# Kernel tuning notes

Measured on AMD Instinct MI355X. Metric: run time of the kernel, lower is better.

The kernel has to match this reference:

```python
import jax, jax.numpy as jnp
import numpy as np

N = 100000
E = 1600000
IN_CH, HID_CH, OUT_CH = 128, 64, 32


def setup_inputs() -> dict:
    key = jax.random.key(0)
    ks = jax.random.split(key, 6)
    x = jax.random.normal(ks[0], (N, IN_CH), dtype=jnp.float32)
    ei = jax.random.randint(ks[1], (2, E), 0, N, dtype=jnp.int64)
    W1 = jax.random.normal(ks[2], (IN_CH, HID_CH), dtype=jnp.float32) * 0.05
    b1 = jax.random.normal(ks[3], (HID_CH,), dtype=jnp.float32) * 0.05
    W2 = jax.random.normal(ks[4], (HID_CH, OUT_CH), dtype=jnp.float32) * 0.05
    b2 = jax.random.normal(ks[5], (OUT_CH,), dtype=jnp.float32) * 0.05
    return {"x": x, "ei": ei, "W1": W1, "b1": b1, "W2": W2, "b2": b2}


def gcn_layer(x, sa, da, n):
    # degree with self-loops already appended in sa/da
    deg = jax.ops.segment_sum(jnp.ones((sa.shape[0],), x.dtype), da, num_segments=n)
    prod = deg[sa] * deg[da]
    norm = jnp.where(prod > 0, jax.lax.rsqrt(prod), 0.0)  # (deg_s*deg_d)^-0.5, inf->0
    msg = x[sa] * norm[:, None]            # [E+N, C] gather + scale
    return jax.ops.segment_sum(msg, da, num_segments=n)  # scatter_add


def reference(x, ei, W1, b1, W2, b2):
    n = x.shape[0]
    loop = jnp.arange(n, dtype=ei.dtype)
    sa = jnp.concatenate([ei[0], loop])
    da = jnp.concatenate([ei[1], loop])
    h = gcn_layer(x @ W1 + b1, sa, da, n)
    h = jax.nn.relu(h)
    # dropout: eval mode (training=False) -> identity
    return gcn_layer(h @ W2 + b2, sa, da, n)
```

## Files before the change

### kernel.cpp

```cpp
#include <hip/hip_runtime.h>

#define NN 100000
#define NE 1600000
#define IN_CH 128
#define HID_CH 64
#define OUT_CH 32
#define NB2 98
#define CHUNKA 8192
#define NBLKA ((NE + CHUNKA - 1) / CHUNKA)
#define NBLK_GEMM ((NN + 63) / 64)

typedef unsigned short ushort_t;
typedef _Float16 half2_t __attribute__((ext_vector_type(2)));
typedef float f32x2 __attribute__((ext_vector_type(2)));

__device__ inline ushort_t f2bf(float f) {
    union { float f; unsigned u; } v; v.f = f;
    unsigned r = v.u + 0x7fff + ((v.u >> 16) & 1);
    return (ushort_t)(r >> 16);
}
__device__ inline float blo(unsigned u) {
    union { unsigned x; float f; } v; v.x = u << 16; return v.f;
}
__device__ inline float bhi(unsigned u) {
    union { unsigned x; float f; } v; v.x = u & 0xffff0000u; return v.f;
}
__device__ inline unsigned pkh(float a, float b) {
    union { half2_t h; unsigned u; } v;
    v.h[0] = (_Float16)a; v.h[1] = (_Float16)b;
    return v.u;
}
__device__ inline half2_t u2h(unsigned u) {
    union { unsigned u; half2_t h; } v; v.u = u; return v.h;
}
__device__ inline float fdot2(unsigned a, unsigned b, float c) {
#if __has_builtin(__builtin_amdgcn_fdot2)
    return __builtin_amdgcn_fdot2(u2h(a), u2h(b), c, false);
#else
    half2_t ha = u2h(a), hb = u2h(b);
    return c + (float)ha[0] * (float)hb[0] + (float)ha[1] * (float)hb[1];
#endif
}
__device__ inline f32x2 pk_add(f32x2 a, f32x2 b) {
    f32x2 r;
    asm("v_pk_add_f32 %0, %1, %2" : "=v"(r) : "v"(a), "v"(b));
    return r;
}

__global__ __launch_bounds__(256) void k_bhist(const int* __restrict__ da,
                                               int* __restrict__ bcnt,
                                               int* __restrict__ bhall) {
    __shared__ int hist[4][NB2];
    int t = threadIdx.x, w = t >> 6;
    for (int i = t; i < 4 * NB2; i += 256) ((int*)hist)[i] = 0;
    __syncthreads();
    int base = blockIdx.x * CHUNKA;
    for (int i = 0; i < CHUNKA; i += 256) {
        int e = base + i + t;
        if (e < NE) atomicAdd(&hist[w][da[e] >> 10], 1);
    }
    __syncthreads();
    if (t < NB2) {
        int c = hist[0][t] + hist[1][t] + hist[2][t] + hist[3][t];
        bhall[blockIdx.x * NB2 + t] = c;
        if (c) atomicAdd(&bcnt[t], c);
    }
}

__global__ __launch_bounds__(128) void k_bscan(const int* __restrict__ bcnt,
                                               int* __restrict__ bbase,
                                               int* __restrict__ bcur,
                                               int* __restrict__ rowptr) {
    __shared__ int lds[128];
    int t = threadIdx.x;
    int v = (t < NB2) ? bcnt[t] : 0;
    lds[t] = v;
    __syncthreads();
    for (int off = 1; off < 128; off <<= 1) {
        int x = (t >= off) ? lds[t - off] : 0;
        __syncthreads();
        lds[t] += x;
        __syncthreads();
    }
    int excl = lds[t] - v;
    if (t < NB2) { bbase[t] = excl; bcur[t] = excl; }
    if (t == 0) { bbase[NB2] = NE; rowptr[NN] = NE; }
}

__global__ __launch_bounds__(256) void k_bfill(const int* __restrict__ sa,
                                               const int* __restrict__ da,
                                               const int* __restrict__ bhall,
                                               int* __restrict__ bcur,
                                               unsigned* __restrict__ ebuf) {
    __shared__ int lcur[NB2];
    int t = threadIdx.x;
    if (t < NB2) {
        int c = bhall[blockIdx.x * NB2 + t];
        lcur[t] = c ? atomicAdd(&bcur[t], c) : 0;
    }
    __syncthreads();
    int base = blockIdx.x * CHUNKA;
    for (int i = 0; i < CHUNKA; i += 256) {
        int e = base + i + t;
        if (e < NE) {
            int d = da[e];
            int p = atomicAdd(&lcur[d >> 10], 1);
            ebuf[p] = ((unsigned)sa[e] << 10) | (unsigned)(d & 1023);
        }
    }
}

__global__ __launch_bounds__(1024) void k_bcount(const unsigned* __restrict__ ebuf,
                                                 const int* __restrict__ bbase,
                                                 int* __restrict__ rowptr,
                                                 float* __restrict__ rs) {
    __shared__ int cnt[1024];
    __shared__ int scn[1024];
    int b = blockIdx.x, t = threadIdx.x;
    int nb = NN - b * 1024; if (nb > 1024) nb = 1024;
    int beg = bbase[b], end = bbase[b + 1];
    cnt[t] = 0;
    __syncthreads();
    for (int i = beg + t; i < end; i += 1024) atomicAdd(&cnt[ebuf[i] & 1023], 1);
    __syncthreads();
    int v = cnt[t];
    scn[t] = v;
    __syncthreads();
    for (int off = 1; off < 1024; off <<= 1) {
        int x = (t >= off) ? scn[t - off] : 0;
        __syncthreads();
        scn[t] += x;
        __syncthreads();
    }
    int excl = scn[t] - v;
    if (t < nb) {
        rowptr[b * 1024 + t] = beg + excl;
        rs[b * 1024 + t] = rsqrtf((float)(v + 1));
    }
}

#define SWZU1(n, k2) ((n) * 64 + ((k2) ^ ((((n) & 7)) << 2)))
#define SWZ2(n, k) ((n) * 64 + ((k) ^ ((((n) & 7)) << 2)))

__global__ __launch_bounds__(256, 4) void k_scatter_gemm1(
    const unsigned* __restrict__ ebuf, const int* __restrict__ rowptr,
    const int* __restrict__ bbase, int* __restrict__ col,
    const float* __restrict__ x, const float* __restrict__ W1,
    const float* __restrict__ b1, const float* __restrict__ rs,
    ushort_t* __restrict__ xsb) {
    __shared__ unsigned xth[64 * 64];
    __shared__ unsigned w1h[64 * 64];
    __shared__ int cur[1024];
    int t = threadIdx.x;

    if (blockIdx.x < NB2) {
        int b = blockIdx.x;
#pragma unroll
        for (int j = 0; j < 4; ++j) {
            int n = b * 1024 + j * 256 + t;
            cur[j * 256 + t] = (n < NN) ? rowptr[n] : 0;
        }
        int beg = bbase[b], end = bbase[b + 1];
        __syncthreads();
        for (int i = beg + t; i < end; i += 256) {
            unsigned w = ebuf[i];
            int pos = atomicAdd(&cur[w & 1023], 1);
            col[pos] = (int)(w >> 10);
        }
        return;
    }

    int base = (blockIdx.x - NB2) * 64;
#pragma unroll
    for (int i = 0; i < 8; ++i) {
        int flat = i * 1024 + t * 4;
        int node = flat >> 7, k0 = flat & 127;
        int gn = base + node;
        float4 v = make_float4(0.f, 0.f, 0.f, 0.f);
        if (gn < NN) v = *(const float4*)(x + (size_t)gn * IN_CH + k0);
        uint2 pk;
        pk.x = pkh(v.x, v.y);
        pk.y = pkh(v.z, v.w);
        *(uint2*)&xth[SWZU1(node, k0 >> 1)] = pk;
    }
#pragma unroll
    for (int i = 0; i < 16; ++i) {
        int idx = i * 256 + t;
        int k2 = idx >> 6, c = idx & 63;
        float f0 = W1[(2 * k2) * 64 + c];
        float f1 = W1[(2 * k2 + 1) * 64 + c];
        w1h[idx] = pkh(f0, f1);
    }
    __syncthreads();

    int tn = t & 15, tc = t >> 4;
    int c0 = tc * 4;
    float acc[4][4];
#pragma unroll
    for (int a = 0; a < 4; ++a)
#pragma unroll
        for (int b = 0; b < 4; ++b) acc[a][b] = 0.f;

    for (int k2 = 0; k2 < 64; k2 += 2) {
        uint2 xu[4];
#pragma unroll
        for (int jn = 0; jn < 4; ++jn)
            xu[jn] = *(uint2*)&xth[SWZU1(tn + jn * 16, k2)];
        uint4 w0 = *(uint4*)&w1h[(k2 + 0) * 64 + c0];
        uint4 w1 = *(uint4*)&w1h[(k2 + 1) * 64 + c0];
        unsigned wq0[4] = {w0.x, w0.y, w0.z, w0.w};
        unsigned wq1[4] = {w1.x, w1.y, w1.z, w1.w};
#pragma unroll
        for (int jn = 0; jn < 4; ++jn)
#pragma unroll
            for (int jc = 0; jc < 4; ++jc) {
                acc[jn][jc] = fdot2(xu[jn].x, wq0[jc], acc[jn][jc]);
                acc[jn][jc] = fdot2(xu[jn].y, wq1[jc], acc[jn][jc]);
            }
    }

    float4 bb = *(const float4*)&b1[c0];
#pragma unroll
    for (int jn = 0; jn < 4; ++jn) {
        int gn = base + tn + jn * 16;
        if (gn < NN) {
            float r = rs[gn];
            uint2 pk;
            pk.x = (unsigned)f2bf((acc[jn][0] + bb.x) * r) |
                   ((unsigned)f2bf((acc[jn][1] + bb.y) * r) << 16);
            pk.y = (unsigned)f2bf((acc[jn][2] + bb.z) * r) |
                   ((unsigned)f2bf((acc[jn][3] + bb.w) * r) << 16);
            *(uint2*)&xsb[(size_t)gn * HID_CH + c0] = pk;
        }
    }
}

#define ADD8PK(v) do { \
    f32x2 w0_, w1_, w2_, w3_; \
    w0_.x = blo((v).x); w0_.y = bhi((v).x); p0 = pk_add(p0, w0_); \
    w1_.x = blo((v).y); w1_.y = bhi((v).y); p1 = pk_add(p1, w1_); \
    w2_.x = blo((v).z); w2_.y = bhi((v).z); p2 = pk_add(p2, w2_); \
    w3_.x = blo((v).w); w3_.y = bhi((v).w); p3 = pk_add(p3, w3_); } while (0)

__global__ __launch_bounds__(256) void k_agg1(
    const int* __restrict__ rowptr, const int* __restrict__ col,
    const ushort_t* __restrict__ xsb, const float* __restrict__ rs,
    ushort_t* __restrict__ hb) {
    int gid = blockIdx.x * blockDim.x + threadIdx.x;
    int n = gid >> 6;
    if (n >= NN) return;
    int lane = threadIdx.x & 63;
    int g = lane >> 3;
    unsigned c0 = (unsigned)(lane & 7) * 8;
    int beg = rowptr[n], end = rowptr[n + 1];

    f32x2 p0 = {0.f, 0.f}, p1 = {0.f, 0.f}, p2 = {0.f, 0.f}, p3 = {0.f, 0.f};
    if (g == 0) {
        uint4 sv = *(const uint4*)&xsb[(unsigned)n * 64u + c0];
        ADD8PK(sv);
    }

    int i = beg;
    for (; i + 16 <= end; i += 16) {
        int s0 = col[i + g];
        int s1 = col[i + 8 + g];
        uint4 v0 = *(const uint4*)&xsb[(unsigned)s0 * 64u + c0];
        uint4 v1 = *(const uint4*)&xsb[(unsigned)s1 * 64u + c0];
        ADD8PK(v0);
        ADD8PK(v1);
    }
    if (i + 8 <= end) {
        int s0 = col[i + g];
        uint4 v0 = *(const uint4*)&xsb[(unsigned)s0 * 64u + c0];
        ADD8PK(v0);
        i += 8;
    }
    int r = end - i;
    if (g < r) {
        int s0 = col[i + g];
        uint4 v0 = *(const uint4*)&xsb[(unsigned)s0 * 64u + c0];
        ADD8PK(v0);
    }

    float a0 = p0.x, a1 = p0.y, a2 = p1.x, a3 = p1.y;
    float a4 = p2.x, a5 = p2.y, a6 = p3.x, a7 = p3.y;
#pragma unroll
    for (int m = 8; m <= 32; m <<= 1) {
        a0 += __shfl_xor(a0, m); a1 += __shfl_xor(a1, m);
        a2 += __shfl_xor(a2, m); a3 += __shfl_xor(a3, m);
        a4 += __shfl_xor(a4, m); a5 += __shfl_xor(a5, m);
        a6 += __shfl_xor(a6, m); a7 += __shfl_xor(a7, m);
    }

    if (g == 0) {
        float rn = rs[n];
        uint4 pk;
        pk.x = (unsigned)f2bf(fmaxf(a0 * rn, 0.f)) |
               ((unsigned)f2bf(fmaxf(a1 * rn, 0.f)) << 16);
        pk.y = (unsigned)f2bf(fmaxf(a2 * rn, 0.f)) |
               ((unsigned)f2bf(fmaxf(a3 * rn, 0.f)) << 16);
        pk.z = (unsigned)f2bf(fmaxf(a4 * rn, 0.f)) |
               ((unsigned)f2bf(fmaxf(a5 * rn, 0.f)) << 16);
        pk.w = (unsigned)f2bf(fmaxf(a6 * rn, 0.f)) |
               ((unsigned)f2bf(fmaxf(a7 * rn, 0.f)) << 16);
        *(uint4*)&hb[(unsigned)n * 64u + c0] = pk;
    }
}

__global__ __launch_bounds__(256) void k_gemm2(
    const ushort_t* __restrict__ hb, const float* __restrict__ W2,
    const float* __restrict__ b2, const float* __restrict__ rs,
    ushort_t* __restrict__ ysb) {
    __shared__ float ht[64 * 64];
    __shared__ float w2s[64 * 32];
    int t = threadIdx.x;
    int base = blockIdx.x * 64;

#pragma unroll
    for (int i = 0; i < 8; ++i) {
        int uidx = i * 256 + t;
        int node = uidx >> 5, k2 = uidx & 31;
        int gn = base + node;
        unsigned u = 0;
        if (gn < NN) u = *(const unsigned*)&hb[(size_t)gn * HID_CH + k2 * 2];
        float2 f; f.x = blo(u); f.y = bhi(u);
        *(float2*)&ht[SWZ2(node, k2 * 2)] = f;
    }
#pragma unroll
    for (int i = 0; i < 2; ++i) {
        int flat = i * 1024 + t * 4;
        *(float4*)&w2s[flat] = *(const float4*)(W2 + flat);
    }
    __syncthreads();

    int tn = t & 15, tc = t >> 4;
    int c0 = tc * 2;
    float acc[4][2];
#pragma unroll
    for (int a = 0; a < 4; ++a) { acc[a][0] = 0.f; acc[a][1] = 0.f; }

    for (int k0 = 0; k0 < 64; k0 += 4) {
        float xq[4][4], wq[4][2];
#pragma unroll
        for (int j = 0; j < 4; ++j)
            *(float2*)&wq[j][0] = *(float2*)&w2s[(k0 + j) * 32 + c0];
#pragma unroll
        for (int jn = 0; jn < 4; ++jn)
            *(float4*)&xq[jn][0] = *(float4*)&ht[SWZ2(tn + jn * 16, k0)];
#pragma unroll
        for (int jn = 0; jn < 4; ++jn)
#pragma unroll
            for (int j = 0; j < 4; ++j) {
                acc[jn][0] = fmaf(xq[jn][j], wq[j][0], acc[jn][0]);
                acc[jn][1] = fmaf(xq[jn][j], wq[j][1], acc[jn][1]);
            }
    }

    float2 bb = *(const float2*)&b2[c0];
#pragma unroll
    for (int jn = 0; jn < 4; ++jn) {
        int gn = base + tn + jn * 16;
        if (gn < NN) {
            float r = rs[gn];
            unsigned pk = (unsigned)f2bf((acc[jn][0] + bb.x) * r) |
                          ((unsigned)f2bf((acc[jn][1] + bb.y) * r) << 16);
            *(unsigned*)&ysb[(size_t)gn * OUT_CH + c0] = pk;
        }
    }
}

__global__ __launch_bounds__(256) void k_agg2(
    const int* __restrict__ rowptr, const int* __restrict__ col,
    const ushort_t* __restrict__ ysb, const float* __restrict__ rs,
    float* __restrict__ out) {
    int gid = blockIdx.x * blockDim.x + threadIdx.x;
    int n = gid >> 6;
    if (n >= NN) return;
    int lane = threadIdx.x & 63;
    int g = lane >> 2;
    unsigned c0 = (unsigned)(lane & 3) * 8;
    int beg = rowptr[n], end = rowptr[n + 1];

    f32x2 p0 = {0.f, 0.f}, p1 = {0.f, 0.f}, p2 = {0.f, 0.f}, p3 = {0.f, 0.f};
    if (g == 0) {
        uint4 sv = *(const uint4*)&ysb[(unsigned)n * 32u + c0];
        ADD8PK(sv);
    }

    int i = beg;
    for (; i + 16 <= end; i += 16) {
        int s0 = col[i + g];
        uint4 v0 = *(const uint4*)&ysb[(unsigned)s0 * 32u + c0];
        ADD8PK(v0);
    }
    int r = end - i;
    if (g < r) {
        int s0 = col[i + g];
        uint4 v0 = *(const uint4*)&ysb[(unsigned)s0 * 32u + c0];
        ADD8PK(v0);
    }

    float a0 = p0.x, a1 = p0.y, a2 = p1.x, a3 = p1.y;
    float a4 = p2.x, a5 = p2.y, a6 = p3.x, a7 = p3.y;
#pragma unroll
    for (int m = 4; m <= 32; m <<= 1) {
        a0 += __shfl_xor(a0, m); a1 += __shfl_xor(a1, m);
        a2 += __shfl_xor(a2, m); a3 += __shfl_xor(a3, m);
        a4 += __shfl_xor(a4, m); a5 += __shfl_xor(a5, m);
        a6 += __shfl_xor(a6, m); a7 += __shfl_xor(a7, m);
    }

    if (g == 0) {
        float rn = rs[n];
        float4 o0, o1;
        o0.x = a0 * rn; o0.y = a1 * rn; o0.z = a2 * rn; o0.w = a3 * rn;
        o1.x = a4 * rn; o1.y = a5 * rn; o1.z = a6 * rn; o1.w = a7 * rn;
        *(float4*)&out[(size_t)n * OUT_CH + c0] = o0;
        *(float4*)&out[(size_t)n * OUT_CH + c0 + 4] = o1;
    }
}

extern "C" void kernel_launch(void* const* d_in, const int* in_sizes, int n_in,
                              void* d_out, int out_size, void* d_ws, size_t ws_size,
                              hipStream_t stream) {
    const float* x  = (const float*)d_in[0];
    const int*   ei = (const int*)d_in[1];
    const float* W1 = (const float*)d_in[2];
    const float* b1 = (const float*)d_in[3];
    const float* W2 = (const float*)d_in[4];
    const float* b2 = (const float*)d_in[5];
    const int* sa = ei;
    const int* da = ei + NE;

    char* ws = (char*)d_ws;
    size_t off = 0;
    auto alloc = [&](size_t bytes) {
        void* p = ws + off;
        off += (bytes + 255) & ~(size_t)255;
        return p;
    };
    int*      bcnt   = (int*)alloc((size_t)NB2 * 4);
    int*      bbase  = (int*)alloc((size_t)(NB2 + 1) * 4);
    int*      bcur   = (int*)alloc((size_t)NB2 * 4);
    int*      bhall  = (int*)alloc((size_t)NBLKA * NB2 * 4);
    int*      rowptr = (int*)alloc((size_t)(NN + 1) * 4);
    float*    rs     = (float*)alloc((size_t)NN * 4);
    unsigned* ebuf   = (unsigned*)alloc((size_t)NE * 4);
    int*      col    = (int*)alloc((size_t)NE * 4);
    ushort_t* xsb    = (ushort_t*)alloc((size_t)NN * HID_CH * 2);
    ushort_t* hb     = (ushort_t*)alloc((size_t)NN * HID_CH * 2);
    ushort_t* ysb    = (ushort_t*)alloc((size_t)NN * OUT_CH * 2);
    float*    outp   = (float*)d_out;

    const int B = 256;
    hipMemsetAsync(bcnt, 0, (size_t)NB2 * 4, stream);
    k_bhist<<<NBLKA, 256, 0, stream>>>(da, bcnt, bhall);
    k_bscan<<<1, 128, 0, stream>>>(bcnt, bbase, bcur, rowptr);
    k_bfill<<<NBLKA, 256, 0, stream>>>(sa, da, bhall, bcur, ebuf);
    k_bcount<<<NB2, 1024, 0, stream>>>(ebuf, bbase, rowptr, rs);
    k_scatter_gemm1<<<NB2 + NBLK_GEMM, 256, 0, stream>>>(ebuf, rowptr, bbase, col,
                                                         x, W1, b1, rs, xsb);
    k_agg1<<<(NN * 64 + B - 1) / B, B, 0, stream>>>(rowptr, col, xsb, rs, hb);
    k_gemm2<<<NBLK_GEMM, 256, 0, stream>>>(hb, W2, b2, rs, ysb);
    k_agg2<<<(NN * 64 + B - 1) / B, B, 0, stream>>>(rowptr, col, ysb, rs, outp);
}
```

Before: 210.1 us.

## Fuse CSR build and GEMM1 into one cooperative persistent kernel with grid syncs

Replaces the histogram, scan, fill, count and scatter/GEMM1 kernels plus the memset with a single cooperative kernel that uses grid-wide syncs between phases and grid-stride virtual blocks. The aim is to remove launch overhead and the inter-kernel gaps of several small kernels. The bucket totals are now recomputed serially by block 0 from the per-chunk histograms, which drops the global atomics on bcnt. Grid syncs add their own cost, and the GEMM phase now runs with a grid limited by occupancy.

```diff
diff --git a/kernel.cpp b/kernel.cpp
--- a/kernel.cpp
+++ b/kernel.cpp
@@ -1,4 +1,7 @@
 #include <hip/hip_runtime.h>
+#include <hip/hip_cooperative_groups.h>
+
+namespace cg = cooperative_groups;
 
 #define NN 100000
 #define NE 1600000
@@ -9,6 +12,7 @@
 #define CHUNKA 8192
 #define NBLKA ((NE + CHUNKA - 1) / CHUNKA)
 #define NBLK_GEMM ((NN + 63) / 64)
+#define NVB5 (NB2 + NBLK_GEMM)
 
 typedef unsigned short ushort_t;
 typedef _Float16 half2_t __attribute__((ext_vector_type(2)));
@@ -47,190 +51,187 @@
     return r;
 }
 
-__global__ __launch_bounds__(256) void k_bhist(const int* __restrict__ da,
-                                               int* __restrict__ bcnt,
-                                               int* __restrict__ bhall) {
-    __shared__ int hist[4][NB2];
-    int t = threadIdx.x, w = t >> 6;
-    for (int i = t; i < 4 * NB2; i += 256) ((int*)hist)[i] = 0;
-    __syncthreads();
-    int base = blockIdx.x * CHUNKA;
-    for (int i = 0; i < CHUNKA; i += 256) {
-        int e = base + i + t;
-        if (e < NE) atomicAdd(&hist[w][da[e] >> 10], 1);
-    }
-    __syncthreads();
-    if (t < NB2) {
-        int c = hist[0][t] + hist[1][t] + hist[2][t] + hist[3][t];
-        bhall[blockIdx.x * NB2 + t] = c;
-        if (c) atomicAdd(&bcnt[t], c);
-    }
-}
-
-__global__ __launch_bounds__(128) void k_bscan(const int* __restrict__ bcnt,
-                                               int* __restrict__ bbase,
-                                               int* __restrict__ bcur,
-                                               int* __restrict__ rowptr) {
-    __shared__ int lds[128];
-    int t = threadIdx.x;
-    int v = (t < NB2) ? bcnt[t] : 0;
-    lds[t] = v;
-    __syncthreads();
-    for (int off = 1; off < 128; off <<= 1) {
-        int x = (t >= off) ? lds[t - off] : 0;
-        __syncthreads();
-        lds[t] += x;
-        __syncthreads();
-    }
-    int excl = lds[t] - v;
-    if (t < NB2) { bbase[t] = excl; bcur[t] = excl; }
-    if (t == 0) { bbase[NB2] = NE; rowptr[NN] = NE; }
-}
-
-__global__ __launch_bounds__(256) void k_bfill(const int* __restrict__ sa,
-                                               const int* __restrict__ da,
-                                               const int* __restrict__ bhall,
-                                               int* __restrict__ bcur,
-                                               unsigned* __restrict__ ebuf) {
-    __shared__ int lcur[NB2];
-    int t = threadIdx.x;
-    if (t < NB2) {
-        int c = bhall[blockIdx.x * NB2 + t];
-        lcur[t] = c ? atomicAdd(&bcur[t], c) : 0;
-    }
-    __syncthreads();
-    int base = blockIdx.x * CHUNKA;
-    for (int i = 0; i < CHUNKA; i += 256) {
-        int e = base + i + t;
-        if (e < NE) {
-            int d = da[e];
-            int p = atomicAdd(&lcur[d >> 10], 1);
-            ebuf[p] = ((unsigned)sa[e] << 10) | (unsigned)(d & 1023);
-        }
-    }
-}
-
-__global__ __launch_bounds__(1024) void k_bcount(const unsigned* __restrict__ ebuf,
-                                                 const int* __restrict__ bbase,
-                                                 int* __restrict__ rowptr,
-                                                 float* __restrict__ rs) {
-    __shared__ int cnt[1024];
-    __shared__ int scn[1024];
-    int b = blockIdx.x, t = threadIdx.x;
-    int nb = NN - b * 1024; if (nb > 1024) nb = 1024;
-    int beg = bbase[b], end = bbase[b + 1];
-    cnt[t] = 0;
-    __syncthreads();
-    for (int i = beg + t; i < end; i += 1024) atomicAdd(&cnt[ebuf[i] & 1023], 1);
-    __syncthreads();
-    int v = cnt[t];
-    scn[t] = v;
-    __syncthreads();
-    for (int off = 1; off < 1024; off <<= 1) {
-        int x = (t >= off) ? scn[t - off] : 0;
-        __syncthreads();
-        scn[t] += x;
-        __syncthreads();
-    }
-    int excl = scn[t] - v;
-    if (t < nb) {
-        rowptr[b * 1024 + t] = beg + excl;
-        rs[b * 1024 + t] = rsqrtf((float)(v + 1));
-    }
-}
-
 #define SWZU1(n, k2) ((n) * 64 + ((k2) ^ ((((n) & 7)) << 2)))
 #define SWZ2(n, k) ((n) * 64 + ((k) ^ ((((n) & 7)) << 2)))
 
-__global__ __launch_bounds__(256, 4) void k_scatter_gemm1(
-    const unsigned* __restrict__ ebuf, const int* __restrict__ rowptr,
-    const int* __restrict__ bbase, int* __restrict__ col,
+__global__ __launch_bounds__(256, 4) void k_mega(
+    const int* __restrict__ sa, const int* __restrict__ da,
+    int* __restrict__ bhall, int* __restrict__ bbase, int* __restrict__ bcur,
+    int* __restrict__ rowptr, float* __restrict__ rs,
+    unsigned* __restrict__ ebuf, int* __restrict__ col,
     const float* __restrict__ x, const float* __restrict__ W1,
-    const float* __restrict__ b1, const float* __restrict__ rs,
-    ushort_t* __restrict__ xsb) {
-    __shared__ unsigned xth[64 * 64];
-    __shared__ unsigned w1h[64 * 64];
-    __shared__ int cur[1024];
+    const float* __restrict__ b1, ushort_t* __restrict__ xsb) {
+    __shared__ int smem[8192];
+    cg::grid_group grid = cg::this_grid();
     int t = threadIdx.x;
 
-    if (blockIdx.x < NB2) {
-        int b = blockIdx.x;
-#pragma unroll
-        for (int j = 0; j < 4; ++j) {
-            int n = b * 1024 + j * 256 + t;
-            cur[j * 256 + t] = (n < NN) ? rowptr[n] : 0;
-        }
-        int beg = bbase[b], end = bbase[b + 1];
-        __syncthreads();
-        for (int i = beg + t; i < end; i += 256) {
-            unsigned w = ebuf[i];
-            int pos = atomicAdd(&cur[w & 1023], 1);
-            col[pos] = (int)(w >> 10);
-        }
-        return;
-    }
-
-    int base = (blockIdx.x - NB2) * 64;
-#pragma unroll
-    for (int i = 0; i < 8; ++i) {
-        int flat = i * 1024 + t * 4;
-        int node = flat >> 7, k0 = flat & 127;
-        int gn = base + node;
-        float4 v = make_float4(0.f, 0.f, 0.f, 0.f);
-        if (gn < NN) v = *(const float4*)(x + (size_t)gn * IN_CH + k0);
-        uint2 pk;
-        pk.x = pkh(v.x, v.y);
-        pk.y = pkh(v.z, v.w);
-        *(uint2*)&xth[SWZU1(node, k0 >> 1)] = pk;
-    }
-#pragma unroll
-    for (int i = 0; i < 16; ++i) {
-        int idx = i * 256 + t;
-        int k2 = idx >> 6, c = idx & 63;
-        float f0 = W1[(2 * k2) * 64 + c];
-        float f1 = W1[(2 * k2 + 1) * 64 + c];
-        w1h[idx] = pkh(f0, f1);
-    }
-    __syncthreads();
-
-    int tn = t & 15, tc = t >> 4;
-    int c0 = tc * 4;
-    float acc[4][4];
-#pragma unroll
-    for (int a = 0; a < 4; ++a)
-#pragma unroll
-        for (int b = 0; b < 4; ++b) acc[a][b] = 0.f;
-
-    for (int k2 = 0; k2 < 64; k2 += 2) {
-        uint2 xu[4];
-#pragma unroll
-        for (int jn = 0; jn < 4; ++jn)
-            xu[jn] = *(uint2*)&xth[SWZU1(tn + jn * 16, k2)];
-        uint4 w0 = *(uint4*)&w1h[(k2 + 0) * 64 + c0];
-        uint4 w1 = *(uint4*)&w1h[(k2 + 1) * 64 + c0];
-        unsigned wq0[4] = {w0.x, w0.y, w0.z, w0.w};
-        unsigned wq1[4] = {w1.x, w1.y, w1.z, w1.w};
-#pragma unroll
-        for (int jn = 0; jn < 4; ++jn)
-#pragma unroll
-            for (int jc = 0; jc < 4; ++jc) {
-                acc[jn][jc] = fdot2(xu[jn].x, wq0[jc], acc[jn][jc]);
-                acc[jn][jc] = fdot2(xu[jn].y, wq1[jc], acc[jn][jc]);
+    for (int vb = blockIdx.x; vb < NBLKA; vb += gridDim.x) {
+        __syncthreads();
+        for (int i = t; i < 4 * NB2; i += 256) smem[i] = 0;
+        __syncthreads();
+        int base = vb * CHUNKA;
+        int w = t >> 6;
+        for (int i = 0; i < CHUNKA; i += 256) {
+            int e = base + i + t;
+            if (e < NE) atomicAdd(&smem[w * NB2 + (da[e] >> 10)], 1);
+        }
+        __syncthreads();
+        if (t < NB2)
+            bhall[vb * NB2 + t] =
+                smem[t] + smem[NB2 + t] + smem[2 * NB2 + t] + smem[3 * NB2 + t];
+        __syncthreads();
+    }
+    grid.sync();
+
+    if (blockIdx.x == 0) {
+        int v = 0;
+        if (t < NB2)
+            for (int r = 0; r < NBLKA; ++r) v += bhall[r * NB2 + t];
+        smem[t] = v;
+        __syncthreads();
+        for (int off = 1; off < 256; off <<= 1) {
+            int xv = (t >= off) ? smem[t - off] : 0;
+            __syncthreads();
+            smem[t] += xv;
+            __syncthreads();
+        }
+        int excl = smem[t] - v;
+        if (t < NB2) { bbase[t] = excl; bcur[t] = excl; }
+        if (t == 0) { bbase[NB2] = NE; rowptr[NN] = NE; }
+    }
+    grid.sync();
+
+    for (int vb = blockIdx.x; vb < NBLKA; vb += gridDim.x) {
+        __syncthreads();
+        if (t < NB2) {
+            int c = bhall[vb * NB2 + t];
+            smem[t] = c ? atomicAdd(&bcur[t], c) : 0;
+        }
+        __syncthreads();
+        int base = vb * CHUNKA;
+        for (int i = 0; i < CHUNKA; i += 256) {
+            int e = base + i + t;
+            if (e < NE) {
+                int d = da[e];
+                int p = atomicAdd(&smem[d >> 10], 1);
+                ebuf[p] = ((unsigned)sa[e] << 10) | (unsigned)(d & 1023);
             }
-    }
-
-    float4 bb = *(const float4*)&b1[c0];
-#pragma unroll
-    for (int jn = 0; jn < 4; ++jn) {
-        int gn = base + tn + jn * 16;
-        if (gn < NN) {
-            float r = rs[gn];
+        }
+    }
+    grid.sync();
+
+    for (int vb = blockIdx.x; vb < NB2; vb += gridDim.x) {
+        __syncthreads();
+        *(int4*)&smem[t * 4] = make_int4(0, 0, 0, 0);
+        __syncthreads();
+        int beg = bbase[vb], end = bbase[vb + 1];
+        for (int i = beg + t; i < end; i += 256)
+            atomicAdd(&smem[ebuf[i] & 1023], 1);
+        __syncthreads();
+        int4 v4 = *(int4*)&smem[t * 4];
+        int s = v4.x + v4.y + v4.z + v4.w;
+        smem[1024 + t] = s;
+        __syncthreads();
+        for (int off = 1; off < 256; off <<= 1) {
+            int xv = (t >= off) ? smem[1024 + t - off] : 0;
+            __syncthreads();
+            smem[1024 + t] += xv;
+            __syncthreads();
+        }
+        int excl = smem[1024 + t] - s;
+        int p0 = beg + excl;
+        int p1 = p0 + v4.x;
+        int p2 = p1 + v4.y;
+        int p3 = p2 + v4.z;
+        int n = vb * 1024 + t * 4;
+        if (n + 0 < NN) { rowptr[n + 0] = p0; rs[n + 0] = rsqrtf((float)(v4.x + 1)); }
+        if (n + 1 < NN) { rowptr[n + 1] = p1; rs[n + 1] = rsqrtf((float)(v4.y + 1)); }
+        if (n + 2 < NN) { rowptr[n + 2] = p2; rs[n + 2] = rsqrtf((float)(v4.z + 1)); }
+        if (n + 3 < NN) { rowptr[n + 3] = p3; rs[n + 3] = rsqrtf((float)(v4.w + 1)); }
+    }
+    grid.sync();
+
+    unsigned* xth = (unsigned*)smem;
+    unsigned* w1h = (unsigned*)smem + 4096;
+    for (int vb = blockIdx.x; vb < NVB5; vb += gridDim.x) {
+        __syncthreads();
+        if (vb < NB2) {
+#pragma unroll
+            for (int j = 0; j < 4; ++j) {
+                int n = vb * 1024 + j * 256 + t;
+                smem[j * 256 + t] = (n < NN) ? rowptr[n] : 0;
+            }
+            int beg = bbase[vb], end = bbase[vb + 1];
+            __syncthreads();
+            for (int i = beg + t; i < end; i += 256) {
+                unsigned w = ebuf[i];
+                int pos = atomicAdd(&smem[w & 1023], 1);
+                col[pos] = (int)(w >> 10);
+            }
+            continue;
+        }
+        int base = (vb - NB2) * 64;
+#pragma unroll
+        for (int i = 0; i < 8; ++i) {
+            int flat = i * 1024 + t * 4;
+            int node = flat >> 7, k0 = flat & 127;
+            int gn = base + node;
+            float4 v = make_float4(0.f, 0.f, 0.f, 0.f);
+            if (gn < NN) v = *(const float4*)(x + (size_t)gn * IN_CH + k0);
             uint2 pk;
-            pk.x = (unsigned)f2bf((acc[jn][0] + bb.x) * r) |
-                   ((unsigned)f2bf((acc[jn][1] + bb.y) * r) << 16);
-            pk.y = (unsigned)f2bf((acc[jn][2] + bb.z) * r) |
-                   ((unsigned)f2bf((acc[jn][3] + bb.w) * r) << 16);
-            *(uint2*)&xsb[(size_t)gn * HID_CH + c0] = pk;
+            pk.x = pkh(v.x, v.y);
+            pk.y = pkh(v.z, v.w);
+            *(uint2*)&xth[SWZU1(node, k0 >> 1)] = pk;
+        }
+#pragma unroll
+        for (int i = 0; i < 16; ++i) {
+            int idx = i * 256 + t;
+            int k2 = idx >> 6, c = idx & 63;
+            float f0 = W1[(2 * k2) * 64 + c];
+            float f1 = W1[(2 * k2 + 1) * 64 + c];
+            w1h[idx] = pkh(f0, f1);
+        }
+        __syncthreads();
+
+        int tn = t & 15, tc = t >> 4;
+        int c0 = tc * 4;
+        float acc[4][4];
+#pragma unroll
+        for (int a = 0; a < 4; ++a)
+#pragma unroll
+            for (int b = 0; b < 4; ++b) acc[a][b] = 0.f;
+
+        for (int k2 = 0; k2 < 64; k2 += 2) {
+            uint2 xu[4];
+#pragma unroll
+            for (int jn = 0; jn < 4; ++jn)
+                xu[jn] = *(uint2*)&xth[SWZU1(tn + jn * 16, k2)];
+            uint4 w0 = *(uint4*)&w1h[(k2 + 0) * 64 + c0];
+            uint4 w1 = *(uint4*)&w1h[(k2 + 1) * 64 + c0];
+            unsigned wq0[4] = {w0.x, w0.y, w0.z, w0.w};
+            unsigned wq1[4] = {w1.x, w1.y, w1.z, w1.w};
+#pragma unroll
+            for (int jn = 0; jn < 4; ++jn)
+#pragma unroll
+                for (int jc = 0; jc < 4; ++jc) {
+                    acc[jn][jc] = fdot2(xu[jn].x, wq0[jc], acc[jn][jc]);
+                    acc[jn][jc] = fdot2(xu[jn].y, wq1[jc], acc[jn][jc]);
+                }
+        }
+
+        float4 bb = *(const float4*)&b1[c0];
+#pragma unroll
+        for (int jn = 0; jn < 4; ++jn) {
+            int gn = base + tn + jn * 16;
+            if (gn < NN) {
+                float r = rs[gn];
+                uint2 pk;
+                pk.x = (unsigned)f2bf((acc[jn][0] + bb.x) * r) |
+                       ((unsigned)f2bf((acc[jn][1] + bb.y) * r) << 16);
+                pk.y = (unsigned)f2bf((acc[jn][2] + bb.z) * r) |
+                       ((unsigned)f2bf((acc[jn][3] + bb.w) * r) << 16);
+                *(uint2*)&xsb[(size_t)gn * HID_CH + c0] = pk;
+            }
         }
     }
 }
@@ -439,7 +440,6 @@
         off += (bytes + 255) & ~(size_t)255;
         return p;
     };
-    int*      bcnt   = (int*)alloc((size_t)NB2 * 4);
     int*      bbase  = (int*)alloc((size_t)(NB2 + 1) * 4);
     int*      bcur   = (int*)alloc((size_t)NB2 * 4);
     int*      bhall  = (int*)alloc((size_t)NBLKA * NB2 * 4);
@@ -453,13 +453,18 @@
     float*    outp   = (float*)d_out;
 
     const int B = 256;
-    hipMemsetAsync(bcnt, 0, (size_t)NB2 * 4, stream);
-    k_bhist<<<NBLKA, 256, 0, stream>>>(da, bcnt, bhall);
-    k_bscan<<<1, 128, 0, stream>>>(bcnt, bbase, bcur, rowptr);
-    k_bfill<<<NBLKA, 256, 0, stream>>>(sa, da, bhall, bcur, ebuf);
-    k_bcount<<<NB2, 1024, 0, stream>>>(ebuf, bbase, rowptr, rs);
-    k_scatter_gemm1<<<NB2 + NBLK_GEMM, 256, 0, stream>>>(ebuf, rowptr, bbase, col,
-                                                         x, W1, b1, rs, xsb);
+
+    int maxBlocksPerCU = 0;
+    hipOccupancyMaxActiveBlocksPerMultiprocessor(&maxBlocksPerCU, k_mega, 256, 0);
+    if (maxBlocksPerCU < 1) maxBlocksPerCU = 1;
+    int nbg = maxBlocksPerCU * 256;
+    if (nbg > NVB5) nbg = NVB5;
+
+    void* args[] = {(void*)&sa, (void*)&da, (void*)&bhall, (void*)&bbase,
+                    (void*)&bcur, (void*)&rowptr, (void*)&rs, (void*)&ebuf,
+                    (void*)&col, (void*)&x, (void*)&W1, (void*)&b1, (void*)&xsb};
+    hipLaunchCooperativeKernel((void*)k_mega, dim3(nbg), dim3(256), args, 0, stream);
+
     k_agg1<<<(NN * 64 + B - 1) / B, B, 0, stream>>>(rowptr, col, xsb, rs, hb);
     k_gemm2<<<NBLK_GEMM, 256, 0, stream>>>(hb, W2, b2, rs, ysb);
     k_agg2<<<(NN * 64 + B - 1) / B, B, 0, stream>>>(rowptr, col, ysb, rs, outp);
```

After: 442.5 us. +110.6%, slower.

## Fuse layer-1 aggregation into GEMM2 and drop bucket-count atomics and memset

Applied to the files above, without the earlier changes.

Merges k_agg1 and k_gemm2 into one kernel. Each block aggregates 64 nodes (one wave handles 16 nodes serially) and writes the ReLU'd fp32 hidden rows into padded LDS, then runs the W2 GEMM from LDS. This removes the bf16 hidden-buffer round trip through global memory and one launch. It also removes the global bucket-count atomics and memset by having the single-block scan sum the per-block histograms. The cost is fewer waves in flight during aggregation (1563 blocks, 16 serial nodes per wave), which may reduce latency hiding for the gather. The scan also now does a serial ~196-iteration sum per thread.

```diff
diff --git a/kernel.cpp b/kernel.cpp
--- a/kernel.cpp
+++ b/kernel.cpp
@@ -9,6 +9,7 @@
 #define CHUNKA 8192
 #define NBLKA ((NE + CHUNKA - 1) / CHUNKA)
 #define NBLK_GEMM ((NN + 63) / 64)
+#define HPAD 68
 
 typedef unsigned short ushort_t;
 typedef _Float16 half2_t __attribute__((ext_vector_type(2)));
@@ -48,7 +49,6 @@
 }
 
 __global__ __launch_bounds__(256) void k_bhist(const int* __restrict__ da,
-                                               int* __restrict__ bcnt,
                                                int* __restrict__ bhall) {
     __shared__ int hist[4][NB2];
     int t = threadIdx.x, w = t >> 6;
@@ -60,20 +60,20 @@
         if (e < NE) atomicAdd(&hist[w][da[e] >> 10], 1);
     }
     __syncthreads();
-    if (t < NB2) {
-        int c = hist[0][t] + hist[1][t] + hist[2][t] + hist[3][t];
-        bhall[blockIdx.x * NB2 + t] = c;
-        if (c) atomicAdd(&bcnt[t], c);
-    }
-}
-
-__global__ __launch_bounds__(128) void k_bscan(const int* __restrict__ bcnt,
+    if (t < NB2)
+        bhall[blockIdx.x * NB2 + t] =
+            hist[0][t] + hist[1][t] + hist[2][t] + hist[3][t];
+}
+
+__global__ __launch_bounds__(128) void k_bscan(const int* __restrict__ bhall,
                                                int* __restrict__ bbase,
                                                int* __restrict__ bcur,
                                                int* __restrict__ rowptr) {
     __shared__ int lds[128];
     int t = threadIdx.x;
-    int v = (t < NB2) ? bcnt[t] : 0;
+    int v = 0;
+    if (t < NB2)
+        for (int r = 0; r < NBLKA; ++r) v += bhall[r * NB2 + t];
     lds[t] = v;
     __syncthreads();
     for (int off = 1; off < 128; off <<= 1) {
@@ -140,7 +140,6 @@
 }
 
 #define SWZU1(n, k2) ((n) * 64 + ((k2) ^ ((((n) & 7)) << 2)))
-#define SWZ2(n, k) ((n) * 64 + ((k) ^ ((((n) & 7)) << 2)))
 
 __global__ __launch_bounds__(256, 4) void k_scatter_gemm1(
     const unsigned* __restrict__ ebuf, const int* __restrict__ rowptr,
@@ -242,99 +241,86 @@
     w2_.x = blo((v).z); w2_.y = bhi((v).z); p2 = pk_add(p2, w2_); \
     w3_.x = blo((v).w); w3_.y = bhi((v).w); p3 = pk_add(p3, w3_); } while (0)
 
-__global__ __launch_bounds__(256) void k_agg1(
+__global__ __launch_bounds__(256) void k_agg1g2(
     const int* __restrict__ rowptr, const int* __restrict__ col,
     const ushort_t* __restrict__ xsb, const float* __restrict__ rs,
-    ushort_t* __restrict__ hb) {
-    int gid = blockIdx.x * blockDim.x + threadIdx.x;
-    int n = gid >> 6;
-    if (n >= NN) return;
-    int lane = threadIdx.x & 63;
-    int g = lane >> 3;
-    unsigned c0 = (unsigned)(lane & 7) * 8;
-    int beg = rowptr[n], end = rowptr[n + 1];
-
-    f32x2 p0 = {0.f, 0.f}, p1 = {0.f, 0.f}, p2 = {0.f, 0.f}, p3 = {0.f, 0.f};
-    if (g == 0) {
-        uint4 sv = *(const uint4*)&xsb[(unsigned)n * 64u + c0];
-        ADD8PK(sv);
-    }
-
-    int i = beg;
-    for (; i + 16 <= end; i += 16) {
-        int s0 = col[i + g];
-        int s1 = col[i + 8 + g];
-        uint4 v0 = *(const uint4*)&xsb[(unsigned)s0 * 64u + c0];
-        uint4 v1 = *(const uint4*)&xsb[(unsigned)s1 * 64u + c0];
-        ADD8PK(v0);
-        ADD8PK(v1);
-    }
-    if (i + 8 <= end) {
-        int s0 = col[i + g];
-        uint4 v0 = *(const uint4*)&xsb[(unsigned)s0 * 64u + c0];
-        ADD8PK(v0);
-        i += 8;
-    }
-    int r = end - i;
-    if (g < r) {
-        int s0 = col[i + g];
-        uint4 v0 = *(const uint4*)&xsb[(unsigned)s0 * 64u + c0];
-        ADD8PK(v0);
-    }
-
-    float a0 = p0.x, a1 = p0.y, a2 = p1.x, a3 = p1.y;
-    float a4 = p2.x, a5 = p2.y, a6 = p3.x, a7 = p3.y;
-#pragma unroll
-    for (int m = 8; m <= 32; m <<= 1) {
-        a0 += __shfl_xor(a0, m); a1 += __shfl_xor(a1, m);
-        a2 += __shfl_xor(a2, m); a3 += __shfl_xor(a3, m);
-        a4 += __shfl_xor(a4, m); a5 += __shfl_xor(a5, m);
-        a6 += __shfl_xor(a6, m); a7 += __shfl_xor(a7, m);
-    }
-
-    if (g == 0) {
-        float rn = rs[n];
-        uint4 pk;
-        pk.x = (unsigned)f2bf(fmaxf(a0 * rn, 0.f)) |
-               ((unsigned)f2bf(fmaxf(a1 * rn, 0.f)) << 16);
-        pk.y = (unsigned)f2bf(fmaxf(a2 * rn, 0.f)) |
-               ((unsigned)f2bf(fmaxf(a3 * rn, 0.f)) << 16);
-        pk.z = (unsigned)f2bf(fmaxf(a4 * rn, 0.f)) |
-               ((unsigned)f2bf(fmaxf(a5 * rn, 0.f)) << 16);
-        pk.w = (unsigned)f2bf(fmaxf(a6 * rn, 0.f)) |
-               ((unsigned)f2bf(fmaxf(a7 * rn, 0.f)) << 16);
-        *(uint4*)&hb[(unsigned)n * 64u + c0] = pk;
-    }
-}
-
-__global__ __launch_bounds__(256) void k_gemm2(
-    const ushort_t* __restrict__ hb, const float* __restrict__ W2,
-    const float* __restrict__ b2, const float* __restrict__ rs,
+    const float* __restrict__ W2, const float* __restrict__ b2,
     ushort_t* __restrict__ ysb) {
-    __shared__ float ht[64 * 64];
+    __shared__ float ht[64 * HPAD];
     __shared__ float w2s[64 * 32];
     int t = threadIdx.x;
     int base = blockIdx.x * 64;
 
 #pragma unroll
-    for (int i = 0; i < 8; ++i) {
-        int uidx = i * 256 + t;
-        int node = uidx >> 5, k2 = uidx & 31;
-        int gn = base + node;
-        unsigned u = 0;
-        if (gn < NN) u = *(const unsigned*)&hb[(size_t)gn * HID_CH + k2 * 2];
-        float2 f; f.x = blo(u); f.y = bhi(u);
-        *(float2*)&ht[SWZ2(node, k2 * 2)] = f;
-    }
-#pragma unroll
     for (int i = 0; i < 2; ++i) {
         int flat = i * 1024 + t * 4;
         *(float4*)&w2s[flat] = *(const float4*)(W2 + flat);
     }
+
+    int wv = t >> 6;
+    int lane = t & 63;
+    int g = lane >> 3;
+    unsigned c0 = (unsigned)(lane & 7) * 8;
+
+    for (int j = 0; j < 16; ++j) {
+        int nl = wv * 16 + j;
+        int n = base + nl;
+        if (n >= NN) break;
+        int beg = rowptr[n], end = rowptr[n + 1];
+
+        f32x2 p0 = {0.f, 0.f}, p1 = {0.f, 0.f}, p2 = {0.f, 0.f}, p3 = {0.f, 0.f};
+        if (g == 0) {
+            uint4 sv = *(const uint4*)&xsb[(unsigned)n * 64u + c0];
+            ADD8PK(sv);
+        }
+
+        int i = beg;
+        for (; i + 16 <= end; i += 16) {
+            int s0 = col[i + g];
+            int s1 = col[i + 8 + g];
+            uint4 v0 = *(const uint4*)&xsb[(unsigned)s0 * 64u + c0];
+            uint4 v1 = *(const uint4*)&xsb[(unsigned)s1 * 64u + c0];
+            ADD8PK(v0);
+            ADD8PK(v1);
+        }
+        if (i + 8 <= end) {
+            int s0 = col[i + g];
+            uint4 v0 = *(const uint4*)&xsb[(unsigned)s0 * 64u + c0];
+            ADD8PK(v0);
+            i += 8;
+        }
+        int r = end - i;
+        if (g < r) {
+            int s0 = col[i + g];
+            uint4 v0 = *(const uint4*)&xsb[(unsigned)s0 * 64u + c0];
+            ADD8PK(v0);
+        }
+
+        float a0 = p0.x, a1 = p0.y, a2 = p1.x, a3 = p1.y;
+        float a4 = p2.x, a5 = p2.y, a6 = p3.x, a7 = p3.y;
+#pragma unroll
+        for (int m = 8; m <= 32; m <<= 1) {
+            a0 += __shfl_xor(a0, m); a1 += __shfl_xor(a1, m);
+            a2 += __shfl_xor(a2, m); a3 += __shfl_xor(a3, m);
+            a4 += __shfl_xor(a4, m); a5 += __shfl_xor(a5, m);
+            a6 += __shfl_xor(a6, m); a7 += __shfl_xor(a7, m);
+        }
+
+        if (g == 0) {
+            float rn = rs[n];
+            float4 h0, h1;
+            h0.x = fmaxf(a0 * rn, 0.f); h0.y = fmaxf(a1 * rn, 0.f);
+            h0.z = fmaxf(a2 * rn, 0.f); h0.w = fmaxf(a3 * rn, 0.f);
+            h1.x = fmaxf(a4 * rn, 0.f); h1.y = fmaxf(a5 * rn, 0.f);
+            h1.z = fmaxf(a6 * rn, 0.f); h1.w = fmaxf(a7 * rn, 0.f);
+            *(float4*)&ht[nl * HPAD + c0] = h0;
+            *(float4*)&ht[nl * HPAD + c0 + 4] = h1;
+        }
+    }
     __syncthreads();
 
     int tn = t & 15, tc = t >> 4;
-    int c0 = tc * 2;
+    int cc0 = tc * 2;
     float acc[4][2];
 #pragma unroll
     for (int a = 0; a < 4; ++a) { acc[a][0] = 0.f; acc[a][1] = 0.f; }
@@ -343,10 +329,10 @@
         float xq[4][4], wq[4][2];
 #pragma unroll
         for (int j = 0; j < 4; ++j)
-            *(float2*)&wq[j][0] = *(float2*)&w2s[(k0 + j) * 32 + c0];
+            *(float2*)&wq[j][0] = *(float2*)&w2s[(k0 + j) * 32 + cc0];
 #pragma unroll
         for (int jn = 0; jn < 4; ++jn)
-            *(float4*)&xq[jn][0] = *(float4*)&ht[SWZ2(tn + jn * 16, k0)];
+            *(float4*)&xq[jn][0] = *(float4*)&ht[(tn + jn * 16) * HPAD + k0];
 #pragma unroll
         for (int jn = 0; jn < 4; ++jn)
 #pragma unroll
@@ -356,7 +342,7 @@
             }
     }
 
-    float2 bb = *(const float2*)&b2[c0];
+    float2 bb = *(const float2*)&b2[cc0];
 #pragma unroll
     for (int jn = 0; jn < 4; ++jn) {
         int gn = base + tn + jn * 16;
@@ -364,7 +350,7 @@
             float r = rs[gn];
             unsigned pk = (unsigned)f2bf((acc[jn][0] + bb.x) * r) |
                           ((unsigned)f2bf((acc[jn][1] + bb.y) * r) << 16);
-            *(unsigned*)&ysb[(size_t)gn * OUT_CH + c0] = pk;
+            *(unsigned*)&ysb[(size_t)gn * OUT_CH + cc0] = pk;
         }
     }
 }
@@ -439,7 +425,6 @@
         off += (bytes + 255) & ~(size_t)255;
         return p;
     };
-    int*      bcnt   = (int*)alloc((size_t)NB2 * 4);
     int*      bbase  = (int*)alloc((size_t)(NB2 + 1) * 4);
     int*      bcur   = (int*)alloc((size_t)NB2 * 4);
     int*      bhall  = (int*)alloc((size_t)NBLKA * NB2 * 4);
@@ -448,19 +433,16 @@
     unsigned* ebuf   = (unsigned*)alloc((size_t)NE * 4);
     int*      col    = (int*)alloc((size_t)NE * 4);
     ushort_t* xsb    = (ushort_t*)alloc((size_t)NN * HID_CH * 2);
-    ushort_t* hb     = (ushort_t*)alloc((size_t)NN * HID_CH * 2);
     ushort_t* ysb    = (ushort_t*)alloc((size_t)NN * OUT_CH * 2);
     float*    outp   = (float*)d_out;
 
     const int B = 256;
-    hipMemsetAsync(bcnt, 0, (size_t)NB2 * 4, stream);
-    k_bhist<<<NBLKA, 256, 0, stream>>>(da, bcnt, bhall);
-    k_bscan<<<1, 128, 0, stream>>>(bcnt, bbase, bcur, rowptr);
+    k_bhist<<<NBLKA, 256, 0, stream>>>(da, bhall);
+    k_bscan<<<1, 128, 0, stream>>>(bhall, bbase, bcur, rowptr);
     k_bfill<<<NBLKA, 256, 0, stream>>>(sa, da, bhall, bcur, ebuf);
     k_bcount<<<NB2, 1024, 0, stream>>>(ebuf, bbase, rowptr, rs);
     k_scatter_gemm1<<<NB2 + NBLK_GEMM, 256, 0, stream>>>(ebuf, rowptr, bbase, col,
                                                          x, W1, b1, rs, xsb);
-    k_agg1<<<(NN * 64 + B - 1) / B, B, 0, stream>>>(rowptr, col, xsb, rs, hb);
-    k_gemm2<<<NBLK_GEMM, 256, 0, stream>>>(hb, W2, b2, rs, ysb);
+    k_agg1g2<<<NBLK_GEMM, 256, 0, stream>>>(rowptr, col, xsb, rs, W2, b2, ysb);
     k_agg2<<<(NN * 64 + B - 1) / B, B, 0, stream>>>(rowptr, col, ysb, rs, outp);
 }
```

After: 353.5 us. 68.2% more time.
